# Performance work log

Hardware: AMD Instinct MI355X
Metric: run time of the kernel (lower is better)

## Reference

```python
import jax, jax.numpy as jnp
import numpy as np

L = 5          # num_layer
D = 256        # emb_dim
N = 50000      # nodes
E = 800000     # edges
NUM_ATOM_FEATS, ATOM_VOCAB = 9, 120
NUM_BOND_FEATS, BOND_VOCAB = 3, 6
BN_EPS = 1e-5


def setup_inputs() -> dict:
    key = jax.random.key(0)
    ks = jax.random.split(key, 16)
    s = 0.02
    inp = {
        "x": jax.random.randint(ks[0], (N, NUM_ATOM_FEATS), 0, ATOM_VOCAB),
        "edge_index": jax.random.randint(ks[1], (2, E), 0, N),
        "edge_attr": jax.random.randint(ks[2], (E, NUM_BOND_FEATS), 0, BOND_VOCAB),
        "atom_emb": jax.random.normal(ks[3], (NUM_ATOM_FEATS, ATOM_VOCAB, D), jnp.float32) * s,
        "bond_emb": jax.random.normal(ks[4], (L, NUM_BOND_FEATS, BOND_VOCAB, D), jnp.float32) * s,
        "eps": jnp.zeros((L,), jnp.float32),
        "W1": jax.random.normal(ks[5], (L, D, 2 * D), jnp.float32) * s,
        "b1": jnp.zeros((L, 2 * D), jnp.float32),
        "g1": jnp.ones((L, 2 * D), jnp.float32),
        "be1": jnp.zeros((L, 2 * D), jnp.float32),
        "W2": jax.random.normal(ks[6], (L, 2 * D, D), jnp.float32) * s,
        "b2": jnp.zeros((L, D), jnp.float32),
        "g2": jnp.ones((L, D), jnp.float32),
        "be2": jnp.zeros((L, D), jnp.float32),
    }
    return inp


def _batchnorm(h, g, b):
    # training-mode BatchNorm1d over the node dimension
    m = jnp.mean(h, axis=0)
    v = jnp.mean(jnp.square(h - m), axis=0)
    return (h - m) * jax.lax.rsqrt(v + BN_EPS) * g + b


def reference(x, edge_index, edge_attr, atom_emb, bond_emb, eps,
              W1, b1, g1, be1, W2, b2, g2, be2):
    # AtomEncoder: sum of per-feature embedding lookups -> [N, D]
    h = jnp.sum(
        jnp.stack([atom_emb[f][x[:, f]] for f in range(NUM_ATOM_FEATS)], 0), 0)
    src, dst = edge_index[0], edge_index[1]
    for l in range(L):
        # BondEncoder for this layer -> [E, D]
        e = jnp.sum(jnp.stack(
            [bond_emb[l, f][edge_attr[:, f]] for f in range(NUM_BOND_FEATS)], 0), 0)
        msg = jax.nn.relu(h[src] + e)                          # gather + transform
        agg = jax.ops.segment_sum(msg, dst, num_segments=N)   # scatter-add
        z = (1.0 + eps[l]) * h + agg
        z = _batchnorm(z @ W1[l] + b1[l], g1[l], be1[l])       # MLP hidden + BN
        z = jax.nn.relu(z) @ W2[l] + b2[l]
        z = _batchnorm(z, g2[l], be2[l])                       # outer BN
        if l < L - 1:
            z = jax.nn.relu(z)
        h = z
    return h  # JK='last', drop_ratio=0
```

## Files before the change

kernel.cpp:

```cpp
#include <hip/hip_runtime.h>
#include <stdint.h>

#define NODES 50000
#define EDGES 800000
#define EMB   256
#define MPAD  50048
#define BNEPS 1e-5f
#define SCANB 196

typedef unsigned short u16;
typedef unsigned int   u32;
typedef _Float16 f16;
typedef __attribute__((ext_vector_type(4))) _Float16 f16x4;
typedef __attribute__((ext_vector_type(8))) _Float16 f16x8;
typedef __attribute__((ext_vector_type(4))) float f32x4;

__device__ __forceinline__ void gload16(const void* g, void* l){
  __builtin_amdgcn_global_load_lds((const __attribute__((address_space(1))) void*)g,
                                   (__attribute__((address_space(3))) void*)l, 16, 0, 0);
}


__global__ void k_w1t(const float* __restrict__ W1, f16* __restrict__ Wt){
  int i = blockIdx.x * 256 + threadIdx.x;
  if (i >= 5*512*256) return;
  int k = i & 255, n = (i >> 8) & 511, l = i >> 17;
  Wt[i] = (f16)W1[((size_t)l << 17) + ((size_t)k << 9) + n];
}
__global__ void k_w2t(const float* __restrict__ W2, f16* __restrict__ Wt){
  int i = blockIdx.x * 256 + threadIdx.x;
  if (i >= 5*256*512) return;
  int k = i & 511, n = (i >> 9) & 255, l = i >> 17;
  Wt[i] = (f16)W2[((size_t)l << 17) + ((size_t)k << 8) + n];
}

__global__ void k_ebond(const float* __restrict__ bemb, f16* __restrict__ eb){
  int l = blockIdx.x / 216, p = blockIdx.x % 216;
  int a0 = p % 6, a1 = (p / 6) % 6, a2 = p / 36;
  int d0 = threadIdx.x * 4;
  const float* b = bemb + (size_t)l * 3 * 6 * 256;
  float4 v0 = *(const float4*)(b + (0*6 + a0)*256 + d0);
  float4 v1 = *(const float4*)(b + (1*6 + a1)*256 + d0);
  float4 v2 = *(const float4*)(b + (2*6 + a2)*256 + d0);
  f16x4 o = {(f16)(v0.x+v1.x+v2.x), (f16)(v0.y+v1.y+v2.y),
             (f16)(v0.z+v1.z+v2.z), (f16)(v0.w+v1.w+v2.w)};
  *(f16x4*)(eb + (((size_t)l*216 + p) << 8) + d0) = o;
}

__global__ void k_atom(const int* __restrict__ x, const float* __restrict__ aemb,
                       f16* __restrict__ h){
  int n = blockIdx.x * 4 + (threadIdx.x >> 6);
  int lane = threadIdx.x & 63;
  if (n >= NODES) return;
  int d0 = lane * 4;
  float a0=0.f, a1=0.f, a2=0.f, a3=0.f;
#pragma unroll
  for (int f = 0; f < 9; ++f){
    int v = x[n*9 + f];
    float4 e = *(const float4*)(aemb + (((size_t)f*120 + v) << 8) + d0);
    a0 += e.x; a1 += e.y; a2 += e.z; a3 += e.w;
  }
  f16x4 o = {(f16)a0, (f16)a1, (f16)a2, (f16)a3};
  *(f16x4*)(h + (size_t)n*EMB + d0) = o;
}


__global__ void k_hist(const int* __restrict__ dst, int* __restrict__ counts){
  int e = blockIdx.x * 256 + threadIdx.x;
  if (e < EDGES) atomicAdd(&counts[dst[e]], 1);
}

__global__ void k_bsum(const int* __restrict__ counts, int* __restrict__ bsums){
  __shared__ int red[256];
  int t = threadIdx.x;
  int i = blockIdx.x * 256 + t;
  red[t] = (i < NODES) ? counts[i] : 0;
  __syncthreads();
  for (int off = 128; off > 0; off >>= 1){
    if (t < off) red[t] += red[t + off];
    __syncthreads();
  }
  if (t == 0) bsums[blockIdx.x] = red[0];
}

__global__ void k_bscan(int* __restrict__ bsums){
  __shared__ int sc[256];
  int t = threadIdx.x;
  int v = (t < SCANB) ? bsums[t] : 0;
  sc[t] = v;
  __syncthreads();
  for (int off = 1; off < 256; off <<= 1){
    int u = (t >= off) ? sc[t - off] : 0;
    __syncthreads();
    sc[t] += u;
    __syncthreads();
  }
  if (t < SCANB) bsums[t] = sc[t] - v;
}

__global__ void k_fill(const int* __restrict__ counts, const int* __restrict__ bsums,
                       int* __restrict__ rs, int* __restrict__ fill){
  __shared__ int sc[256];
  int t = threadIdx.x;
  int i = blockIdx.x * 256 + t;
  int v = (i < NODES) ? counts[i] : 0;
  sc[t] = v;
  __syncthreads();
  for (int off = 1; off < 256; off <<= 1){
    int u = (t >= off) ? sc[t - off] : 0;
    __syncthreads();
    sc[t] += u;
    __syncthreads();
  }
  if (i < NODES){
    int e = bsums[blockIdx.x] + sc[t] - v;
    rs[i] = e; fill[i] = e;
    if (i == NODES - 1) rs[NODES] = e + v;
  }
}

__global__ void k_scatter(const int* __restrict__ src, const int* __restrict__ dst,
                          const int* __restrict__ ea, int* __restrict__ fill,
                          int* __restrict__ csrc, int* __restrict__ cattr){
  int e = blockIdx.x * 256 + threadIdx.x;
  if (e >= EDGES) return;
  int d = dst[e];
  int p = atomicAdd(&fill[d], 1);
  csrc[p]  = src[e];
  cattr[p] = ea[e*3+0] + 6*ea[e*3+1] + 36*ea[e*3+2];
}


__global__ void k_gather(const f16* __restrict__ h, const f16* __restrict__ ebl,
                         const int* __restrict__ rs, const int* __restrict__ csrc,
                         const int* __restrict__ cattr, const float* __restrict__ epsv,
                         int layer, f16* __restrict__ z){
  int n = blockIdx.x * 4 + (threadIdx.x >> 6);
  int lane = threadIdx.x & 63;
  int half = lane >> 5;
  int dl = (lane & 31) * 8;
  if (n >= MPAD) return;
  if (n >= NODES){
    if (half == 0){
      f16x8 zz = {(f16)0.f,(f16)0.f,(f16)0.f,(f16)0.f,(f16)0.f,(f16)0.f,(f16)0.f,(f16)0.f};
      *(f16x8*)(z + (size_t)n*EMB + dl) = zz;
    }
    return;
  }
  float acc[8];
#pragma unroll
  for (int k = 0; k < 8; ++k) acc[k] = 0.f;
  int i1 = rs[n+1];
  int i  = rs[n] + half;
  bool v = i < i1;
  int s = 0, pa = 0;
  if (v){ s = csrc[i]; pa = cattr[i]; }
  while (v){
    f16x8 hv = *(const f16x8*)(h + (size_t)s*EMB + dl);
    f16x8 ev = *(const f16x8*)(ebl + ((size_t)pa << 8) + dl);
    int in = i + 2;
    bool vn = in < i1;
    int sn = 0, pan = 0;
    if (vn){ sn = csrc[in]; pan = cattr[in]; }
#pragma unroll
    for (int k = 0; k < 8; ++k)
      acc[k] += fmaxf((float)hv[k] + (float)ev[k], 0.f);
    i = in; s = sn; pa = pan; v = vn;
  }
#pragma unroll
  for (int k = 0; k < 8; ++k) acc[k] += __shfl_xor(acc[k], 32);
  if (half == 0){
    float ep = 1.0f + epsv[layer];
    f16x8 hv = *(const f16x8*)(h + (size_t)n*EMB + dl);
    f16x8 o;
#pragma unroll
    for (int k = 0; k < 8; ++k) o[k] = (f16)(acc[k] + ep*(float)hv[k]);
    *(f16x8*)(z + (size_t)n*EMB + dl) = o;
  }
}

template<int K, int NCOL>
__global__ __launch_bounds__(256)
void k_gemm(const f16* __restrict__ A, const f16* __restrict__ Bt,
            f16* __restrict__ C, float* __restrict__ csum, float* __restrict__ csq){
  __shared__ __align__(16) u16 As[128*64];
  __shared__ __align__(16) u16 Bs[128*64];
  const int tid  = threadIdx.x;
  const int lane = tid & 63;
  const int wid  = tid >> 6;
  const int bm0 = blockIdx.x * 128;
  const int bn0 = blockIdx.y * 128;
  const int wm = (wid >> 1) * 64;
  const int wn = (wid & 1) * 64;

  f32x4 acc[4][4];
#pragma unroll
  for (int m = 0; m < 4; ++m)
#pragma unroll
    for (int n = 0; n < 4; ++n) acc[m][n] = (f32x4){0.f,0.f,0.f,0.f};

  for (int kt = 0; kt < K/64; ++kt){
    __syncthreads();
#pragma unroll
    for (int it = 0; it < 4; ++it){
      int tix = tid + it*256;
      int r = tix >> 3;
      int c = tix & 7;
      int sc = c ^ (r & 7);
      gload16(A  + (size_t)(bm0 + r)*K + kt*64 + sc*8, (char*)As + tix*16);
      gload16(Bt + (size_t)(bn0 + r)*K + kt*64 + sc*8, (char*)Bs + tix*16);
    }
    __syncthreads();
#pragma unroll
    for (int kk = 0; kk < 2; ++kk){
      f16x8 af[4], bfr[4];
#pragma unroll
      for (int m = 0; m < 4; ++m){
        int row = wm + m*16 + (lane & 15);
        int phys = (kk*4 + (lane >> 4)) ^ (row & 7);
        af[m] = *(const f16x8*)((const char*)As + row*128 + phys*16);
      }
#pragma unroll
      for (int n = 0; n < 4; ++n){
        int row = wn + n*16 + (lane & 15);
        int phys = (kk*4 + (lane >> 4)) ^ (row & 7);
        bfr[n] = *(const f16x8*)((const char*)Bs + row*128 + phys*16);
      }
#pragma unroll
      for (int m = 0; m < 4; ++m)
#pragma unroll
        for (int n = 0; n < 4; ++n)
          acc[m][n] = __builtin_amdgcn_mfma_f32_16x16x32_f16(af[m], bfr[n], acc[m][n], 0, 0, 0);
    }
  }

  const int r0 = (lane >> 4) * 4;
  const int cc = lane & 15;
#pragma unroll
  for (int m = 0; m < 4; ++m)
#pragma unroll
    for (int n = 0; n < 4; ++n)
#pragma unroll
      for (int j = 0; j < 4; ++j){
        int row = bm0 + wm + m*16 + r0 + j;
        int col = bn0 + wn + n*16 + cc;
        C[(size_t)row*NCOL + col] = (f16)acc[m][n][j];
      }
#pragma unroll
  for (int n = 0; n < 4; ++n){
    float s = 0.f, q = 0.f;
#pragma unroll
    for (int m = 0; m < 4; ++m)
#pragma unroll
      for (int j = 0; j < 4; ++j){ float v = acc[m][n][j]; s += v; q += v*v; }
    s += __shfl_xor(s, 16); q += __shfl_xor(q, 16);
    s += __shfl_xor(s, 32); q += __shfl_xor(q, 32);
    if (lane < 16){
      atomicAdd(csum + bn0 + wn + n*16 + cc, s);
      atomicAdd(csq  + bn0 + wn + n*16 + cc, q);
    }
  }
}

__global__ void k_finalize(const float* __restrict__ sum, const float* __restrict__ sumsq,
                           const float* __restrict__ g, const float* __restrict__ be,
                           float* __restrict__ scale, float* __restrict__ shift, int nc){
  int c = blockIdx.x * 256 + threadIdx.x;
  if (c >= nc) return;
  float m = sum[c] * (1.0f / NODES);
  float v = sumsq[c] * (1.0f / NODES) - m*m;
  float sc = rsqrtf(v + BNEPS) * g[c];
  scale[c] = sc;
  shift[c] = be[c] - m*sc;
}

__global__ void k_apply1(f16* __restrict__ hid, const float* __restrict__ scale,
                         const float* __restrict__ shift){
  int idx = blockIdx.x * 256 + threadIdx.x;
  int row = idx >> 6;
  int c0  = (idx & 63) * 8;
  f16* p = hid + (size_t)row * 512 + c0;
  if (row >= NODES){
    f16x8 zz = {(f16)0.f,(f16)0.f,(f16)0.f,(f16)0.f,(f16)0.f,(f16)0.f,(f16)0.f,(f16)0.f};
    *(f16x8*)p = zz;
    return;
  }
  f16x8 v = *(const f16x8*)p;
  float4 sA = *(const float4*)(scale + c0), sB = *(const float4*)(scale + c0 + 4);
  float4 tA = *(const float4*)(shift + c0), tB = *(const float4*)(shift + c0 + 4);
  f16x8 o;
  o[0] = (f16)fmaxf((float)v[0]*sA.x + tA.x, 0.f);
  o[1] = (f16)fmaxf((float)v[1]*sA.y + tA.y, 0.f);
  o[2] = (f16)fmaxf((float)v[2]*sA.z + tA.z, 0.f);
  o[3] = (f16)fmaxf((float)v[3]*sA.w + tA.w, 0.f);
  o[4] = (f16)fmaxf((float)v[4]*sB.x + tB.x, 0.f);
  o[5] = (f16)fmaxf((float)v[5]*sB.y + tB.y, 0.f);
  o[6] = (f16)fmaxf((float)v[6]*sB.z + tB.z, 0.f);
  o[7] = (f16)fmaxf((float)v[7]*sB.w + tB.w, 0.f);
  *(f16x8*)p = o;
}

__global__ void k_apply2(const f16* __restrict__ zp, const float* __restrict__ scale,
                         const float* __restrict__ shift, f16* __restrict__ hout,
                         float* __restrict__ fout, int dorelu){
  int idx = blockIdx.x * 256 + threadIdx.x;
  int row = idx >> 5;
  int c0  = (idx & 31) * 8;
  if (row >= NODES) return;
  size_t off = (size_t)row * EMB + c0;
  f16x8 v = *(const f16x8*)(zp + off);
  float4 sA = *(const float4*)(scale + c0), sB = *(const float4*)(scale + c0 + 4);
  float4 tA = *(const float4*)(shift + c0), tB = *(const float4*)(shift + c0 + 4);
  float r0 = (float)v[0]*sA.x + tA.x;
  float r1 = (float)v[1]*sA.y + tA.y;
  float r2 = (float)v[2]*sA.z + tA.z;
  float r3 = (float)v[3]*sA.w + tA.w;
  float r4 = (float)v[4]*sB.x + tB.x;
  float r5 = (float)v[5]*sB.y + tB.y;
  float r6 = (float)v[6]*sB.z + tB.z;
  float r7 = (float)v[7]*sB.w + tB.w;
  if (dorelu){
    r0=fmaxf(r0,0.f); r1=fmaxf(r1,0.f); r2=fmaxf(r2,0.f); r3=fmaxf(r3,0.f);
    r4=fmaxf(r4,0.f); r5=fmaxf(r5,0.f); r6=fmaxf(r6,0.f); r7=fmaxf(r7,0.f);
  }
  if (fout){
    float4 f0 = {r0,r1,r2,r3}, f1 = {r4,r5,r6,r7};
    float* q = fout + off;
    *(float4*)q = f0; *(float4*)(q + 4) = f1;
  } else {
    f16x8 o = {(f16)r0,(f16)r1,(f16)r2,(f16)r3,(f16)r4,(f16)r5,(f16)r6,(f16)r7};
    *(f16x8*)(hout + off) = o;
  }
}


extern "C" void kernel_launch(void* const* d_in, const int* in_sizes, int n_in,
                              void* d_out, int out_size, void* d_ws, size_t ws_size,
                              hipStream_t stream){
  const int*   x    = (const int*)  d_in[0];
  const int*   ei   = (const int*)  d_in[1];
  const int*   ea   = (const int*)  d_in[2];
  const float* aemb = (const float*)d_in[3];
  const float* bemb = (const float*)d_in[4];
  const float* epsv = (const float*)d_in[5];
  const float* W1   = (const float*)d_in[6];
  const float* g1   = (const float*)d_in[8];
  const float* be1  = (const float*)d_in[9];
  const float* W2   = (const float*)d_in[10];
  const float* g2   = (const float*)d_in[12];
  const float* be2  = (const float*)d_in[13];
  float* out = (float*)d_out;

  char* p = (char*)d_ws;
  auto take = [&](size_t bytes){ char* r = p; p += (bytes + 255) & ~(size_t)255; return r; };
  f16* h      = (f16*)take((size_t)NODES*EMB*2);
  f16* z      = (f16*)take((size_t)MPAD*EMB*2);
  f16* hidden = (f16*)take((size_t)MPAD*512*2);
  f16* W1t    = (f16*)take((size_t)5*512*256*2);
  f16* W2t    = (f16*)take((size_t)5*256*512*2);
  f16* eb     = (f16*)take((size_t)5*216*256*2);
  float* stats= (float*)take((size_t)4*512*4);
  float* csum = stats, *csq = stats + 512, *scale = stats + 1024, *shift = stats + 1536;
  int* counts = (int*)take((size_t)NODES*4);
  int* rs     = (int*)take((size_t)(NODES+1)*4);
  int* fill   = (int*)take((size_t)NODES*4);
  int* bsums  = (int*)take((size_t)SCANB*4);
  int* csrc   = (int*)take((size_t)EDGES*4);
  int* cattr  = (int*)take((size_t)EDGES*4);

  k_w1t<<<2560, 256, 0, stream>>>(W1, W1t);
  k_w2t<<<2560, 256, 0, stream>>>(W2, W2t);
  k_ebond<<<5*216, 64, 0, stream>>>(bemb, eb);
  k_atom<<<12500, 256, 0, stream>>>(x, aemb, h);
  hipMemsetAsync(counts, 0, (size_t)NODES*4, stream);
  k_hist<<<EDGES/256, 256, 0, stream>>>(ei + EDGES, counts);
  k_bsum<<<SCANB, 256, 0, stream>>>(counts, bsums);
  k_bscan<<<1, 256, 0, stream>>>(bsums);
  k_fill<<<SCANB, 256, 0, stream>>>(counts, bsums, rs, fill);
  k_scatter<<<EDGES/256, 256, 0, stream>>>(ei, ei + EDGES, ea, fill, csrc, cattr);

  for (int l = 0; l < 5; ++l){
    k_gather<<<MPAD/4, 256, 0, stream>>>(h, eb + (size_t)l*216*256, rs, csrc, cattr, epsv, l, z);
    hipMemsetAsync(stats, 0, 2*512*4, stream);
    k_gemm<256,512><<<dim3(MPAD/128, 4), 256, 0, stream>>>(z, W1t + (size_t)l*512*256, hidden, csum, csq);
    k_finalize<<<2, 256, 0, stream>>>(csum, csq, g1 + l*512, be1 + l*512, scale, shift, 512);
    k_apply1<<<MPAD*64/256, 256, 0, stream>>>(hidden, scale, shift);
    hipMemsetAsync(stats, 0, 2*512*4, stream);
    k_gemm<512,256><<<dim3(MPAD/128, 2), 256, 0, stream>>>(hidden, W2t + (size_t)l*256*512, z, csum, csq);
    k_finalize<<<1, 256, 0, stream>>>(csum, csq, g2 + l*256, be2 + l*256, scale, shift, 256);
    if (l < 4)
      k_apply2<<<NODES*32/256, 256, 0, stream>>>(z, scale, shift, h, nullptr, 1);
    else
      k_apply2<<<NODES*32/256, 256, 0, stream>>>(z, scale, shift, nullptr, out, 0);
  }
}
```

Before: 1.242 ms.

## Fuse BN1+ReLU into second GEMM A-load and drop LDS staging

Removes the separate apply1 pass over the 512-wide hidden activations. The hidden-layer batchnorm scale/shift and ReLU are now applied in fp16 registers as the second GEMM loads its A operand, with padded rows masked to zero. The GEMM also stops staging tiles through LDS with global_load_lds and instead loads MFMA fragments straight from global memory. That loses cross-wave reuse within a block and depends on the cache for repeated A/B loads. BN is now applied in fp16 arithmetic rather than fp32, which slightly changes precision.

```diff
diff --git a/kernel.cpp b/kernel.cpp
--- a/kernel.cpp
+++ b/kernel.cpp
@@ -14,11 +14,6 @@
 typedef __attribute__((ext_vector_type(4))) _Float16 f16x4;
 typedef __attribute__((ext_vector_type(8))) _Float16 f16x8;
 typedef __attribute__((ext_vector_type(4))) float f32x4;
-
-__device__ __forceinline__ void gload16(const void* g, void* l){
-  __builtin_amdgcn_global_load_lds((const __attribute__((address_space(1))) void*)g,
-                                   (__attribute__((address_space(3))) void*)l, 16, 0, 0);
-}
 
 
 __global__ void k_w1t(const float* __restrict__ W1, f16* __restrict__ Wt){
@@ -179,12 +174,11 @@
   }
 }
 
-template<int K, int NCOL>
+template<int K, int NCOL, bool FUSEBN>
 __global__ __launch_bounds__(256)
 void k_gemm(const f16* __restrict__ A, const f16* __restrict__ Bt,
+            const f16* __restrict__ bnsc, const f16* __restrict__ bnsh,
             f16* __restrict__ C, float* __restrict__ csum, float* __restrict__ csq){
-  __shared__ __align__(16) u16 As[128*64];
-  __shared__ __align__(16) u16 Bs[128*64];
   const int tid  = threadIdx.x;
   const int lane = tid & 63;
   const int wid  = tid >> 6;
@@ -192,6 +186,11 @@
   const int bn0 = blockIdx.y * 128;
   const int wm = (wid >> 1) * 64;
   const int wn = (wid & 1) * 64;
+  const int lr = lane & 15;
+  const int kc = (lane >> 4) * 8;
+
+  const f16* Ap = A  + (size_t)(bm0 + wm + lr)*K + kc;
+  const f16* Bp = Bt + (size_t)(bn0 + wn + lr)*K + kc;
 
   f32x4 acc[4][4];
 #pragma unroll
@@ -199,39 +198,34 @@
 #pragma unroll
     for (int n = 0; n < 4; ++n) acc[m][n] = (f32x4){0.f,0.f,0.f,0.f};
 
-  for (int kt = 0; kt < K/64; ++kt){
-    __syncthreads();
-#pragma unroll
-    for (int it = 0; it < 4; ++it){
-      int tix = tid + it*256;
-      int r = tix >> 3;
-      int c = tix & 7;
-      int sc = c ^ (r & 7);
-      gload16(A  + (size_t)(bm0 + r)*K + kt*64 + sc*8, (char*)As + tix*16);
-      gload16(Bt + (size_t)(bn0 + r)*K + kt*64 + sc*8, (char*)Bs + tix*16);
+  const f16x8 zero8 = {(f16)0.f,(f16)0.f,(f16)0.f,(f16)0.f,
+                       (f16)0.f,(f16)0.f,(f16)0.f,(f16)0.f};
+
+#pragma unroll 2
+  for (int kk = 0; kk < K/32; ++kk){
+    f16x8 af[4], bf[4];
+#pragma unroll
+    for (int m = 0; m < 4; ++m)
+      af[m] = *(const f16x8*)(Ap + (size_t)m*16*K + kk*32);
+#pragma unroll
+    for (int n = 0; n < 4; ++n)
+      bf[n] = *(const f16x8*)(Bp + (size_t)n*16*K + kk*32);
+    if (FUSEBN){
+      f16x8 sc = *(const f16x8*)(bnsc + kk*32 + kc);
+      f16x8 sh = *(const f16x8*)(bnsh + kk*32 + kc);
+#pragma unroll
+      for (int m = 0; m < 4; ++m){
+        f16x8 t = af[m]*sc + sh;
+#pragma unroll
+        for (int j = 0; j < 8; ++j) t[j] = (t[j] > (f16)0.f) ? t[j] : (f16)0.f;
+        af[m] = (bm0 + wm + m*16 + lr < NODES) ? t : zero8;
+      }
     }
-    __syncthreads();
-#pragma unroll
-    for (int kk = 0; kk < 2; ++kk){
-      f16x8 af[4], bfr[4];
-#pragma unroll
-      for (int m = 0; m < 4; ++m){
-        int row = wm + m*16 + (lane & 15);
-        int phys = (kk*4 + (lane >> 4)) ^ (row & 7);
-        af[m] = *(const f16x8*)((const char*)As + row*128 + phys*16);
-      }
-#pragma unroll
-      for (int n = 0; n < 4; ++n){
-        int row = wn + n*16 + (lane & 15);
-        int phys = (kk*4 + (lane >> 4)) ^ (row & 7);
-        bfr[n] = *(const f16x8*)((const char*)Bs + row*128 + phys*16);
-      }
-#pragma unroll
-      for (int m = 0; m < 4; ++m)
-#pragma unroll
-        for (int n = 0; n < 4; ++n)
-          acc[m][n] = __builtin_amdgcn_mfma_f32_16x16x32_f16(af[m], bfr[n], acc[m][n], 0, 0, 0);
-    }
+#pragma unroll
+    for (int m = 0; m < 4; ++m)
+#pragma unroll
+      for (int n = 0; n < 4; ++n)
+        acc[m][n] = __builtin_amdgcn_mfma_f32_16x16x32_f16(af[m], bf[n], acc[m][n], 0, 0, 0);
   }
 
   const int r0 = (lane >> 4) * 4;
@@ -264,40 +258,16 @@
 
 __global__ void k_finalize(const float* __restrict__ sum, const float* __restrict__ sumsq,
                            const float* __restrict__ g, const float* __restrict__ be,
-                           float* __restrict__ scale, float* __restrict__ shift, int nc){
+                           float* __restrict__ scale, float* __restrict__ shift,
+                           f16* __restrict__ scf, f16* __restrict__ shf, int nc){
   int c = blockIdx.x * 256 + threadIdx.x;
   if (c >= nc) return;
   float m = sum[c] * (1.0f / NODES);
   float v = sumsq[c] * (1.0f / NODES) - m*m;
   float sc = rsqrtf(v + BNEPS) * g[c];
-  scale[c] = sc;
-  shift[c] = be[c] - m*sc;
-}
-
-__global__ void k_apply1(f16* __restrict__ hid, const float* __restrict__ scale,
-                         const float* __restrict__ shift){
-  int idx = blockIdx.x * 256 + threadIdx.x;
-  int row = idx >> 6;
-  int c0  = (idx & 63) * 8;
-  f16* p = hid + (size_t)row * 512 + c0;
-  if (row >= NODES){
-    f16x8 zz = {(f16)0.f,(f16)0.f,(f16)0.f,(f16)0.f,(f16)0.f,(f16)0.f,(f16)0.f,(f16)0.f};
-    *(f16x8*)p = zz;
-    return;
-  }
-  f16x8 v = *(const f16x8*)p;
-  float4 sA = *(const float4*)(scale + c0), sB = *(const float4*)(scale + c0 + 4);
-  float4 tA = *(const float4*)(shift + c0), tB = *(const float4*)(shift + c0 + 4);
-  f16x8 o;
-  o[0] = (f16)fmaxf((float)v[0]*sA.x + tA.x, 0.f);
-  o[1] = (f16)fmaxf((float)v[1]*sA.y + tA.y, 0.f);
-  o[2] = (f16)fmaxf((float)v[2]*sA.z + tA.z, 0.f);
-  o[3] = (f16)fmaxf((float)v[3]*sA.w + tA.w, 0.f);
-  o[4] = (f16)fmaxf((float)v[4]*sB.x + tB.x, 0.f);
-  o[5] = (f16)fmaxf((float)v[5]*sB.y + tB.y, 0.f);
-  o[6] = (f16)fmaxf((float)v[6]*sB.z + tB.z, 0.f);
-  o[7] = (f16)fmaxf((float)v[7]*sB.w + tB.w, 0.f);
-  *(f16x8*)p = o;
+  float sh = be[c] - m*sc;
+  scale[c] = sc;  shift[c] = sh;
+  scf[c] = (f16)sc;  shf[c] = (f16)sh;
 }
 
 __global__ void k_apply2(const f16* __restrict__ zp, const float* __restrict__ scale,
@@ -361,6 +331,8 @@
   f16* eb     = (f16*)take((size_t)5*216*256*2);
   float* stats= (float*)take((size_t)4*512*4);
   float* csum = stats, *csq = stats + 512, *scale = stats + 1024, *shift = stats + 1536;
+  f16* scf    = (f16*)take((size_t)512*2);
+  f16* shf    = (f16*)take((size_t)512*2);
   int* counts = (int*)take((size_t)NODES*4);
   int* rs     = (int*)take((size_t)(NODES+1)*4);
   int* fill   = (int*)take((size_t)NODES*4);
@@ -382,12 +354,15 @@
   for (int l = 0; l < 5; ++l){
     k_gather<<<MPAD/4, 256, 0, stream>>>(h, eb + (size_t)l*216*256, rs, csrc, cattr, epsv, l, z);
     hipMemsetAsync(stats, 0, 2*512*4, stream);
-    k_gemm<256,512><<<dim3(MPAD/128, 4), 256, 0, stream>>>(z, W1t + (size_t)l*512*256, hidden, csum, csq);
-    k_finalize<<<2, 256, 0, stream>>>(csum, csq, g1 + l*512, be1 + l*512, scale, shift, 512);
-    k_apply1<<<MPAD*64/256, 256, 0, stream>>>(hidden, scale, shift);
+    k_gemm<256,512,false><<<dim3(MPAD/128, 4), 256, 0, stream>>>(
+        z, W1t + (size_t)l*512*256, nullptr, nullptr, hidden, csum, csq);
+    k_finalize<<<2, 256, 0, stream>>>(csum, csq, g1 + l*512, be1 + l*512,
+                                      scale, shift, scf, shf, 512);
     hipMemsetAsync(stats, 0, 2*512*4, stream);
-    k_gemm<512,256><<<dim3(MPAD/128, 2), 256, 0, stream>>>(hidden, W2t + (size_t)l*256*512, z, csum, csq);
-    k_finalize<<<1, 256, 0, stream>>>(csum, csq, g2 + l*256, be2 + l*256, scale, shift, 256);
+    k_gemm<512,256,true><<<dim3(MPAD/128, 2), 256, 0, stream>>>(
+        hidden, W2t + (size_t)l*256*512, scf, shf, z, csum, csq);
+    k_finalize<<<1, 256, 0, stream>>>(csum, csq, g2 + l*256, be2 + l*256,
+                                      scale, shift, scf, shf, 256);
     if (l < 4)
       k_apply2<<<NODES*32/256, 256, 0, stream>>>(z, scale, shift, h, nullptr, 1);
     else
```

Result: slower. 1.424 ms (+14.7%).
